# Kernel optimization log

Hardware: AMD Instinct MI355X
Metric: run time of the kernel (lower is better)

The kernel has to match this reference:

```python
import jax, jax.numpy as jnp
import numpy as np

N_VOCAB = 50000
V_SUPPORT = 20000
D = 300
H = 512
B = 8192


def setup_inputs() -> dict:
    key = jax.random.key(0)
    ks = jax.random.split(key, 8)
    ws = jax.random.randint(ks[0], (B,), 0, N_VOCAB, dtype=jnp.int64 if jax.config.jax_enable_x64 else jnp.int32)
    cs = jax.random.randint(ks[1], (B,), 0, N_VOCAB, dtype=ws.dtype)
    vectors = jax.random.normal(ks[2], (N_VOCAB, D), dtype=jnp.float32)
    W1 = jax.random.normal(ks[3], (D, H), dtype=jnp.float32) * (1.0 / np.sqrt(D))
    b1 = jnp.zeros((H,), dtype=jnp.float32)
    W2 = jax.random.normal(ks[4], (H, V_SUPPORT), dtype=jnp.float32) * (1.0 / np.sqrt(H))
    b2 = jnp.zeros((V_SUPPORT,), dtype=jnp.float32)
    vector_to_support = jax.random.randint(ks[5], (N_VOCAB,), 0, V_SUPPORT, dtype=ws.dtype)
    return {"ws": ws, "cs": cs, "vectors": vectors, "W1": W1, "b1": b1,
            "W2": W2, "b2": b2, "vector_to_support": vector_to_support}


def reference(ws, cs, vectors, W1, b1, W2, b2, vector_to_support):
    # embedding lookup of context vectors: [B, D]
    v_c = vectors[cs]
    # FeedForward: Linear -> ReLU -> Linear, then LogSoftmax over support
    h = jax.nn.relu(v_c @ W1 + b1)            # [B, H]
    logits = h @ W2 + b2                       # [B, V]
    logp = jax.nn.log_softmax(logits, axis=-1) # [B, V]
    # map target word (vocab index) -> support index, gather per-row logprob.
    # Original does outputs.T[idx].diag() (O(B^2)); the fused equivalent is a
    # per-row gather: logp[arange(B), idx].
    w_sup = vector_to_support[ws]              # [B]
    logprobs = jnp.take_along_axis(logp, w_sup[:, None], axis=-1)[:, 0]
    return -logprobs                            # [B] NLL per example
```

## Files before the change

kernel.cpp:

```cpp
#include <hip/hip_runtime.h>
#include <hip/hip_bf16.h>
#include <hip/hip_fp8.h>
#include <math.h>


typedef __bf16 bf16x8 __attribute__((ext_vector_type(8)));
typedef float f32x4 __attribute__((ext_vector_type(4)));
typedef int i32x4 __attribute__((ext_vector_type(4)));
typedef int i32x8 __attribute__((ext_vector_type(8)));

#define B_N 8192
#define D_N 300
#define K1K 320
#define H_N 512
#define V_N 20000
#define V_PAD 20480
#define NSPLIT 16
#define SPLIT_V 1280
#define NCH 40
#define ROWS_BLK 128
#define CHUNK_BYTES 16384

#define OFF_PART (8388608u)
#define OFF_W1T  (OFF_PART + 16u*8192u*8u)
#define OFF_B2L  (OFF_W1T + 512u*320u*2u)
#define OFF_H8   (OFF_B2L + 20480u*4u)
#define OFF_W2T8 (OFF_H8 + 8192u*512u)

#define SCALE1 0x7F7F7F7F
#define LOG2E  1.4426950408889634f

__device__ inline unsigned short f2bf(float f) {
  __hip_bfloat16 h = __float2bfloat16(f);
  return *reinterpret_cast<unsigned short*>(&h);
}

__device__ inline unsigned char f2fp8(float f) {
  __hip_fp8_e4m3 q(f);
  return (unsigned char)q.__x;
}

__device__ inline float fp82f(unsigned char b) {
  __hip_fp8_e4m3 q; q.__x = b;
  return (float)q;
}

__device__ __forceinline__ void gl16(const void* g, void* l) {
  __builtin_amdgcn_global_load_lds(
      (const __attribute__((address_space(1))) void*)g,
      (__attribute__((address_space(3))) void*)l, 16, 0, 0);
}

__global__ __launch_bounds__(256) void kprep(
    const float* __restrict__ W2, unsigned long long* __restrict__ W2T8u,
    const float* __restrict__ W1, unsigned int* __restrict__ W1Tu,
    const float* __restrict__ b2, float* __restrict__ b2l)
{
  __shared__ float tile[64][65];
  const int bid = blockIdx.x;
  const int tid = threadIdx.x;

  if (bid < 2560) {
    const int n0 = (bid >> 3) * 64;
    const int k0 = (bid & 7) * 64;
    #pragma unroll
    for (int it = 0; it < 16; ++it) {
      int idx = it * 256 + tid;
      int i = idx >> 6;
      int j = idx & 63;
      float v = 0.f;
      if (n0 + j < V_N) v = W2[(size_t)(k0 + i) * V_N + n0 + j];
      tile[i][j] = v;
    }
    __syncthreads();
    #pragma unroll
    for (int it = 0; it < 2; ++it) {
      int idx = it * 256 + tid;
      int nl = idx >> 3;
      int g8 = (idx & 7) * 8;
      int n = n0 + nl;
      unsigned long long pack = 0;
      #pragma unroll
      for (int j = 0; j < 8; ++j)
        pack |= (unsigned long long)f2fp8(tile[g8 + j][nl]) << (8 * j);
      unsigned kk = (unsigned)(k0 + g8);
      unsigned off = ((unsigned)n * 512u + (kk ^ (((unsigned)n & 15u) << 4)));
      W2T8u[off >> 3] = pack;
    }
  } else if (bid < 2600) {
    const int idx0 = bid - 2560;
    const int n0 = (idx0 & 7) * 64;
    const int k0 = (idx0 >> 3) * 64;
    #pragma unroll
    for (int it = 0; it < 16; ++it) {
      int idx = it * 256 + tid;
      int i = idx >> 6;
      int j = idx & 63;
      float v = 0.f;
      if (k0 + i < D_N) v = W1[(size_t)(k0 + i) * H_N + n0 + j];
      tile[i][j] = v;
    }
    __syncthreads();
    #pragma unroll
    for (int it = 0; it < 8; ++it) {
      int idx = it * 256 + tid;
      int nl = idx >> 5;
      int k = (idx & 31) * 2;
      unsigned int lo = f2bf(tile[k][nl]);
      unsigned int hi = f2bf(tile[k + 1][nl]);
      W1Tu[((size_t)(n0 + nl) * K1K + k0 + k) >> 1] = (hi << 16) | lo;
    }
  } else {
    int i = (bid - 2600) * 256 + tid;
    if (i < V_PAD) b2l[i] = (i < V_N) ? b2[i] * LOG2E : -3.0e37f;
  }
}

__global__ __launch_bounds__(256) void k1_hidden(
    const int* __restrict__ cs, const float* __restrict__ vectors,
    const unsigned short* __restrict__ W1T,
    const float* __restrict__ b1, unsigned char* __restrict__ h8Out)
{
  __shared__ __align__(16) unsigned short vca[16][328];
  __shared__ int rowIdx[16];
  const int tid = threadIdx.x;
  const int lane = tid & 63;
  const int w = tid >> 6;
  const int l15 = lane & 15;
  const int l4 = lane >> 4;
  const int r0 = blockIdx.x * 16;
  if (tid < 16) rowIdx[tid] = cs[r0 + tid];
  __syncthreads();
  for (int idx = tid; idx < 16 * 328; idx += 256) {
    int r = idx / 328;
    int k = idx - r * 328;
    float v = (k < D_N) ? vectors[(size_t)rowIdx[r] * D_N + k] : 0.f;
    vca[r][k] = f2bf(v);
  }
  __syncthreads();

  bf16x8 afr[10];
  #pragma unroll
  for (int t = 0; t < 10; ++t)
    afr[t] = *(const bf16x8*)&vca[l15][t * 32 + l4 * 8];

  f32x4 acc[8];
  #pragma unroll
  for (int ct = 0; ct < 8; ++ct) acc[ct] = (f32x4){0.f, 0.f, 0.f, 0.f};

  #pragma unroll
  for (int t = 0; t < 10; ++t) {
    #pragma unroll
    for (int ct = 0; ct < 8; ++ct) {
      const int n = w * 128 + ct * 16 + l15;
      bf16x8 bfr = *(const bf16x8*)(W1T + (size_t)n * K1K + t * 32 + l4 * 8);
      acc[ct] = __builtin_amdgcn_mfma_f32_16x16x32_bf16(afr[t], bfr, acc[ct], 0, 0, 0);
    }
  }

  #pragma unroll
  for (int ct = 0; ct < 8; ++ct) {
    const int n = w * 128 + ct * 16 + l15;
    const float bb = b1[n];
    #pragma unroll
    for (int r = 0; r < 4; ++r) {
      const int row = r0 + l4 * 4 + r;
      h8Out[(size_t)row * H_N + n] = f2fp8(fmaxf(acc[ct][r] + bb, 0.f));
    }
  }
}

__device__ __forceinline__ void stage_chunk(const char* g, char* l, int tid) {
  #pragma unroll
  for (int it = 0; it < 4; ++it) {
    const unsigned o = (unsigned)tid * 16 + it * 4096;
    gl16(g + o, l + o);
  }
}

__global__ __launch_bounds__(256, 4) void k3_fused(
    const unsigned char* __restrict__ h8,
    const char* __restrict__ W2T8,
    const float* __restrict__ b2l,
    float2* __restrict__ partOut)
{
  __shared__ __align__(16) char smB[2 * CHUNK_BYTES];
  __shared__ float b2s[SPLIT_V];
  const int tid = threadIdx.x;
  const int lane = tid & 63;
  const int w = tid >> 6;
  const int l15 = lane & 15;
  const int l4 = lane >> 4;
  const int s = blockIdx.x & 15;
  const int rb = blockIdx.x >> 4;
  const int r0 = rb * ROWS_BLK + w * 32;
  const char* gsplit = W2T8 + (size_t)s * SPLIT_V * 512;
  const int sCol = s * SPLIT_V;

  i32x8 afr[2][4];
  #pragma unroll
  for (int m = 0; m < 2; ++m) {
    const unsigned char* ap = h8 + (size_t)(r0 + m * 16 + l15) * H_N + l4 * 32;
    #pragma unroll
    for (int t = 0; t < 4; ++t) {
      i32x4 lo = *(const i32x4*)(ap + t * 128);
      i32x4 hi = *(const i32x4*)(ap + t * 128 + 16);
      afr[m][t] = __builtin_shufflevector(lo, hi, 0, 1, 2, 3, 4, 5, 6, 7);
    }
  }

  float s_run[8];
  #pragma unroll
  for (int ri = 0; ri < 8; ++ri) s_run[ri] = 0.f;

  for (int i = tid; i < SPLIT_V; i += 256) b2s[i] = b2l[sCol + i];

  stage_chunk(gsplit, smB, tid);

  const unsigned swz = (unsigned)l15 << 4;

  #pragma unroll 1
  for (int c = 0; c < NCH; ++c) {
    asm volatile("s_waitcnt vmcnt(0) lgkmcnt(0)" ::: "memory");
    __builtin_amdgcn_s_barrier();

    char* cur = smB + (c & 1) * CHUNK_BYTES;
    if (c + 1 < NCH)
      stage_chunk(gsplit + (size_t)(c + 1) * CHUNK_BYTES,
                  smB + ((c & 1) ^ 1) * CHUNK_BYTES, tid);

    const float b2c0 = b2s[c * 32 + l15];
    const float b2c1 = b2s[c * 32 + 16 + l15];

    f32x4 acc[2][2];
    #pragma unroll
    for (int m = 0; m < 2; ++m)
      #pragma unroll
      for (int ct = 0; ct < 2; ++ct) acc[m][ct] = (f32x4){0.f, 0.f, 0.f, 0.f};

    #pragma unroll
    for (int t = 0; t < 4; ++t) {
      const char* bp = cur + l15 * 512;
      i32x4 lo = *(const i32x4*)(bp + (((unsigned)(t * 128 + l4 * 32)) ^ swz));
      i32x4 hi = *(const i32x4*)(bp + (((unsigned)(t * 128 + l4 * 32 + 16)) ^ swz));
      i32x8 bfr = __builtin_shufflevector(lo, hi, 0, 1, 2, 3, 4, 5, 6, 7);
      __builtin_amdgcn_s_setprio(1);
      acc[0][0] = __builtin_amdgcn_mfma_scale_f32_16x16x128_f8f6f4(
          afr[0][t], bfr, acc[0][0], 0, 0, 0, SCALE1, 0, SCALE1);
      acc[1][0] = __builtin_amdgcn_mfma_scale_f32_16x16x128_f8f6f4(
          afr[1][t], bfr, acc[1][0], 0, 0, 0, SCALE1, 0, SCALE1);
      __builtin_amdgcn_s_setprio(0);
    }

    #pragma unroll
    for (int t = 0; t < 4; ++t) {
      const char* bp = cur + (16 + l15) * 512;
      i32x4 lo = *(const i32x4*)(bp + (((unsigned)(t * 128 + l4 * 32)) ^ swz));
      i32x4 hi = *(const i32x4*)(bp + (((unsigned)(t * 128 + l4 * 32 + 16)) ^ swz));
      i32x8 bfr = __builtin_shufflevector(lo, hi, 0, 1, 2, 3, 4, 5, 6, 7);
      __builtin_amdgcn_s_setprio(1);
      acc[0][1] = __builtin_amdgcn_mfma_scale_f32_16x16x128_f8f6f4(
          afr[0][t], bfr, acc[0][1], 0, 0, 0, SCALE1, 0, SCALE1);
      acc[1][1] = __builtin_amdgcn_mfma_scale_f32_16x16x128_f8f6f4(
          afr[1][t], bfr, acc[1][1], 0, 0, 0, SCALE1, 0, SCALE1);
      __builtin_amdgcn_s_setprio(0);
      #pragma unroll
      for (int r2 = 0; r2 < 2; ++r2) {
        const int ri = t * 2 + r2;
        const int m_ = ri >> 2, r_ = ri & 3;
        s_run[ri] += __builtin_amdgcn_exp2f(fmaf(acc[m_][0][r_], LOG2E, b2c0));
      }
    }

    #pragma unroll
    for (int m = 0; m < 2; ++m)
      #pragma unroll
      for (int r = 0; r < 4; ++r)
        s_run[m * 4 + r] += __builtin_amdgcn_exp2f(fmaf(acc[m][1][r], LOG2E, b2c1));
  }

  #pragma unroll
  for (int m = 0; m < 2; ++m)
    #pragma unroll
    for (int r = 0; r < 4; ++r) {
      int ri = m * 4 + r;
      float sc = s_run[ri];
      #pragma unroll
      for (int k = 1; k < 16; k <<= 1) sc += __shfl_xor(sc, k);
      if (l15 == 0) {
        int grow = r0 + m * 16 + l4 * 4 + r;
        partOut[(size_t)s * B_N + grow] = make_float2(0.f, sc);
      }
    }
}

__global__ __launch_bounds__(256) void k45_final(
    const unsigned char* __restrict__ h8, const char* __restrict__ W2T8,
    const float* __restrict__ b2, const int* __restrict__ wsIdx,
    const int* __restrict__ v2s, const float2* __restrict__ part,
    float* __restrict__ out)
{
  const int row = blockIdx.x * 4 + (threadIdx.x >> 6);
  const int lane = threadIdx.x & 63;
  const int tc = v2s[wsIdx[row]];
  unsigned long long hv = *(const unsigned long long*)(h8 + (size_t)row * H_N + lane * 8);
  const unsigned off = ((unsigned)(lane * 8)) ^ (((unsigned)tc & 15u) << 4);
  unsigned long long wv = *(const unsigned long long*)(W2T8 + (size_t)tc * 512 + off);
  float sdot = 0.f;
  #pragma unroll
  for (int j = 0; j < 8; ++j)
    sdot += fp82f((unsigned char)(hv >> (8 * j))) * fp82f((unsigned char)(wv >> (8 * j)));
  #pragma unroll
  for (int k = 32; k >= 1; k >>= 1) sdot += __shfl_xor(sdot, k);
  if (lane == 0) {
    const float tgt = sdot + b2[tc];
    float S = 0.f;
    #pragma unroll
    for (int s = 0; s < NSPLIT; ++s) S += part[(size_t)s * B_N + row].y;
    out[row] = logf(S) - tgt;
  }
}

extern "C" void kernel_launch(void* const* d_in, const int* in_sizes, int n_in,
                              void* d_out, int out_size, void* d_ws, size_t ws_size,
                              hipStream_t stream) {
  const int*   wsIdx   = (const int*)d_in[0];
  const int*   cs      = (const int*)d_in[1];
  const float* vectors = (const float*)d_in[2];
  const float* W1      = (const float*)d_in[3];
  const float* b1      = (const float*)d_in[4];
  const float* W2      = (const float*)d_in[5];
  const float* b2      = (const float*)d_in[6];
  const int*   v2s     = (const int*)d_in[7];

  char* wsb = (char*)d_ws;
  float2* part = (float2*)(wsb + OFF_PART);
  unsigned short* W1T = (unsigned short*)(wsb + OFF_W1T);
  float*  b2l  = (float*)(wsb + OFF_B2L);
  unsigned char* h8   = (unsigned char*)(wsb + OFF_H8);
  char*   W2T8 = wsb + OFF_W2T8;
  float*  out  = (float*)d_out;

  hipLaunchKernelGGL(kprep, dim3(2680), dim3(256), 0, stream,
                     W2, (unsigned long long*)W2T8, W1, (unsigned int*)W1T, b2, b2l);
  hipLaunchKernelGGL(k1_hidden, dim3(B_N / 16), dim3(256), 0, stream, cs, vectors, W1T, b1, h8);
  hipLaunchKernelGGL(k3_fused, dim3((B_N / ROWS_BLK) * NSPLIT), dim3(256), 0, stream,
                     h8, W2T8, b2l, part);
  hipLaunchKernelGGL(k45_final, dim3(B_N / 4), dim3(256), 0, stream,
                     h8, W2T8, b2, wsIdx, v2s, part, out);
}
```

Measured before the change: 123.9 us.

## Read W2 fp8 fragments directly from global memory instead of LDS staging

```diff
diff --git a/kernel.cpp b/kernel.cpp
--- a/kernel.cpp
+++ b/kernel.cpp
@@ -19,7 +19,6 @@
 #define SPLIT_V 1280
 #define NCH 40
 #define ROWS_BLK 128
-#define CHUNK_BYTES 16384
 
 #define OFF_PART (8388608u)
 #define OFF_W1T  (OFF_PART + 16u*8192u*8u)
@@ -43,12 +42,6 @@
 __device__ inline float fp82f(unsigned char b) {
   __hip_fp8_e4m3 q; q.__x = b;
   return (float)q;
-}
-
-__device__ __forceinline__ void gl16(const void* g, void* l) {
-  __builtin_amdgcn_global_load_lds(
-      (const __attribute__((address_space(1))) void*)g,
-      (__attribute__((address_space(3))) void*)l, 16, 0, 0);
 }
 
 __global__ __launch_bounds__(256) void kprep(
@@ -83,8 +76,7 @@
       #pragma unroll
       for (int j = 0; j < 8; ++j)
         pack |= (unsigned long long)f2fp8(tile[g8 + j][nl]) << (8 * j);
-      unsigned kk = (unsigned)(k0 + g8);
-      unsigned off = ((unsigned)n * 512u + (kk ^ (((unsigned)n & 15u) << 4)));
+      unsigned off = ((unsigned)n * 512u + (unsigned)(k0 + g8));
       W2T8u[off >> 3] = pack;
     }
   } else if (bid < 2600) {
@@ -170,22 +162,12 @@
   }
 }
 
-__device__ __forceinline__ void stage_chunk(const char* g, char* l, int tid) {
-  #pragma unroll
-  for (int it = 0; it < 4; ++it) {
-    const unsigned o = (unsigned)tid * 16 + it * 4096;
-    gl16(g + o, l + o);
-  }
-}
-
 __global__ __launch_bounds__(256, 4) void k3_fused(
     const unsigned char* __restrict__ h8,
     const char* __restrict__ W2T8,
     const float* __restrict__ b2l,
     float2* __restrict__ partOut)
 {
-  __shared__ __align__(16) char smB[2 * CHUNK_BYTES];
-  __shared__ float b2s[SPLIT_V];
   const int tid = threadIdx.x;
   const int lane = tid & 63;
   const int w = tid >> 6;
@@ -194,7 +176,6 @@
   const int s = blockIdx.x & 15;
   const int rb = blockIdx.x >> 4;
   const int r0 = rb * ROWS_BLK + w * 32;
-  const char* gsplit = W2T8 + (size_t)s * SPLIT_V * 512;
   const int sCol = s * SPLIT_V;
 
   i32x8 afr[2][4];
@@ -213,24 +194,15 @@
   #pragma unroll
   for (int ri = 0; ri < 8; ++ri) s_run[ri] = 0.f;
 
-  for (int i = tid; i < SPLIT_V; i += 256) b2s[i] = b2l[sCol + i];
-
-  stage_chunk(gsplit, smB, tid);
-
-  const unsigned swz = (unsigned)l15 << 4;
+  const char* bbase = W2T8 + (size_t)(sCol + l15) * 512 + l4 * 32;
 
   #pragma unroll 1
   for (int c = 0; c < NCH; ++c) {
-    asm volatile("s_waitcnt vmcnt(0) lgkmcnt(0)" ::: "memory");
-    __builtin_amdgcn_s_barrier();
-
-    char* cur = smB + (c & 1) * CHUNK_BYTES;
-    if (c + 1 < NCH)
-      stage_chunk(gsplit + (size_t)(c + 1) * CHUNK_BYTES,
-                  smB + ((c & 1) ^ 1) * CHUNK_BYTES, tid);
-
-    const float b2c0 = b2s[c * 32 + l15];
-    const float b2c1 = b2s[c * 32 + 16 + l15];
+    const float b2c0 = b2l[sCol + c * 32 + l15];
+    const float b2c1 = b2l[sCol + c * 32 + 16 + l15];
+
+    const char* bp0 = bbase + (size_t)(c * 32) * 512;
+    const char* bp1 = bp0 + 16 * 512;
 
     f32x4 acc[2][2];
     #pragma unroll
@@ -240,9 +212,8 @@
 
     #pragma unroll
     for (int t = 0; t < 4; ++t) {
-      const char* bp = cur + l15 * 512;
-      i32x4 lo = *(const i32x4*)(bp + (((unsigned)(t * 128 + l4 * 32)) ^ swz));
-      i32x4 hi = *(const i32x4*)(bp + (((unsigned)(t * 128 + l4 * 32 + 16)) ^ swz));
+      i32x4 lo = *(const i32x4*)(bp0 + t * 128);
+      i32x4 hi = *(const i32x4*)(bp0 + t * 128 + 16);
       i32x8 bfr = __builtin_shufflevector(lo, hi, 0, 1, 2, 3, 4, 5, 6, 7);
       __builtin_amdgcn_s_setprio(1);
       acc[0][0] = __builtin_amdgcn_mfma_scale_f32_16x16x128_f8f6f4(
@@ -254,9 +225,8 @@
 
     #pragma unroll
     for (int t = 0; t < 4; ++t) {
-      const char* bp = cur + (16 + l15) * 512;
-      i32x4 lo = *(const i32x4*)(bp + (((unsigned)(t * 128 + l4 * 32)) ^ swz));
-      i32x4 hi = *(const i32x4*)(bp + (((unsigned)(t * 128 + l4 * 32 + 16)) ^ swz));
+      i32x4 lo = *(const i32x4*)(bp1 + t * 128);
+      i32x4 hi = *(const i32x4*)(bp1 + t * 128 + 16);
       i32x8 bfr = __builtin_shufflevector(lo, hi, 0, 1, 2, 3, 4, 5, 6, 7);
       __builtin_amdgcn_s_setprio(1);
       acc[0][1] = __builtin_amdgcn_mfma_scale_f32_16x16x128_f8f6f4(
@@ -304,8 +274,7 @@
   const int lane = threadIdx.x & 63;
   const int tc = v2s[wsIdx[row]];
   unsigned long long hv = *(const unsigned long long*)(h8 + (size_t)row * H_N + lane * 8);
-  const unsigned off = ((unsigned)(lane * 8)) ^ (((unsigned)tc & 15u) << 4);
-  unsigned long long wv = *(const unsigned long long*)(W2T8 + (size_t)tc * 512 + off);
+  unsigned long long wv = *(const unsigned long long*)(W2T8 + (size_t)tc * 512 + lane * 8);
   float sdot = 0.f;
   #pragma unroll
   for (int j = 0; j < 8; ++j)
```

Result: slower. 340.3 us (+174.6%).

## Load second half of W2 chunk directly into registers from fragment-ordered copy

Applied to the files above, without the earlier changes.

```diff
diff --git a/kernel.cpp b/kernel.cpp
--- a/kernel.cpp
+++ b/kernel.cpp
@@ -20,7 +20,9 @@
 #define NCH 40
 #define ROWS_BLK 128
 #define CHUNK_BYTES 16384
-
+#define STG_BYTES 8192
+
+#define OFF_W2F  0u
 #define OFF_PART (8388608u)
 #define OFF_W1T  (OFF_PART + 16u*8192u*8u)
 #define OFF_B2L  (OFF_W1T + 512u*320u*2u)
@@ -53,6 +55,7 @@
 
 __global__ __launch_bounds__(256) void kprep(
     const float* __restrict__ W2, unsigned long long* __restrict__ W2T8u,
+    unsigned long long* __restrict__ W2Fu,
     const float* __restrict__ W1, unsigned int* __restrict__ W1Tu,
     const float* __restrict__ b2, float* __restrict__ b2l)
 {
@@ -86,6 +89,14 @@
       unsigned kk = (unsigned)(k0 + g8);
       unsigned off = ((unsigned)n * 512u + (kk ^ (((unsigned)n & 15u) << 4)));
       W2T8u[off >> 3] = pack;
+      if (n & 16) {
+        unsigned sc = (unsigned)n >> 5;
+        unsigned t  = kk >> 7;
+        unsigned l4 = (kk >> 5) & 3;
+        unsigned lanei = l4 * 16 + ((unsigned)n & 15);
+        unsigned foff = (((sc * 4 + t) * 64) + lanei) * 32 + (kk & 31);
+        W2Fu[foff >> 3] = pack;
+      }
     }
   } else if (bid < 2600) {
     const int idx0 = bid - 2560;
@@ -170,9 +181,9 @@
   }
 }
 
-__device__ __forceinline__ void stage_chunk(const char* g, char* l, int tid) {
-  #pragma unroll
-  for (int it = 0; it < 4; ++it) {
+__device__ __forceinline__ void stage_half(const char* g, char* l, int tid) {
+  #pragma unroll
+  for (int it = 0; it < 2; ++it) {
     const unsigned o = (unsigned)tid * 16 + it * 4096;
     gl16(g + o, l + o);
   }
@@ -181,10 +192,11 @@
 __global__ __launch_bounds__(256, 4) void k3_fused(
     const unsigned char* __restrict__ h8,
     const char* __restrict__ W2T8,
+    const char* __restrict__ W2F,
     const float* __restrict__ b2l,
     float2* __restrict__ partOut)
 {
-  __shared__ __align__(16) char smB[2 * CHUNK_BYTES];
+  __shared__ __align__(16) char smB[2 * STG_BYTES];
   __shared__ float b2s[SPLIT_V];
   const int tid = threadIdx.x;
   const int lane = tid & 63;
@@ -195,6 +207,7 @@
   const int rb = blockIdx.x >> 4;
   const int r0 = rb * ROWS_BLK + w * 32;
   const char* gsplit = W2T8 + (size_t)s * SPLIT_V * 512;
+  const char* fsplit = W2F + ((size_t)s * NCH * 4 * 64) * 32 + (size_t)lane * 32;
   const int sCol = s * SPLIT_V;
 
   i32x8 afr[2][4];
@@ -215,7 +228,7 @@
 
   for (int i = tid; i < SPLIT_V; i += 256) b2s[i] = b2l[sCol + i];
 
-  stage_chunk(gsplit, smB, tid);
+  stage_half(gsplit, smB, tid);
 
   const unsigned swz = (unsigned)l15 << 4;
 
@@ -224,10 +237,20 @@
     asm volatile("s_waitcnt vmcnt(0) lgkmcnt(0)" ::: "memory");
     __builtin_amdgcn_s_barrier();
 
-    char* cur = smB + (c & 1) * CHUNK_BYTES;
+    const char* fb = fsplit + (size_t)(c * 4) * 2048;
+    i32x4 dlo0 = *(const i32x4*)(fb);
+    i32x4 dhi0 = *(const i32x4*)(fb + 16);
+    i32x4 dlo1 = *(const i32x4*)(fb + 2048);
+    i32x4 dhi1 = *(const i32x4*)(fb + 2048 + 16);
+    i32x4 dlo2 = *(const i32x4*)(fb + 2 * 2048);
+    i32x4 dhi2 = *(const i32x4*)(fb + 2 * 2048 + 16);
+    i32x4 dlo3 = *(const i32x4*)(fb + 3 * 2048);
+    i32x4 dhi3 = *(const i32x4*)(fb + 3 * 2048 + 16);
+
+    char* cur = smB + (c & 1) * STG_BYTES;
     if (c + 1 < NCH)
-      stage_chunk(gsplit + (size_t)(c + 1) * CHUNK_BYTES,
-                  smB + ((c & 1) ^ 1) * CHUNK_BYTES, tid);
+      stage_half(gsplit + (size_t)(c + 1) * CHUNK_BYTES,
+                 smB + ((c & 1) ^ 1) * STG_BYTES, tid);
 
     const float b2c0 = b2s[c * 32 + l15];
     const float b2c1 = b2s[c * 32 + 16 + l15];
@@ -254,9 +277,8 @@
 
     #pragma unroll
     for (int t = 0; t < 4; ++t) {
-      const char* bp = cur + (16 + l15) * 512;
-      i32x4 lo = *(const i32x4*)(bp + (((unsigned)(t * 128 + l4 * 32)) ^ swz));
-      i32x4 hi = *(const i32x4*)(bp + (((unsigned)(t * 128 + l4 * 32 + 16)) ^ swz));
+      i32x4 lo = (t == 0) ? dlo0 : (t == 1) ? dlo1 : (t == 2) ? dlo2 : dlo3;
+      i32x4 hi = (t == 0) ? dhi0 : (t == 1) ? dhi1 : (t == 2) ? dhi2 : dhi3;
       i32x8 bfr = __builtin_shufflevector(lo, hi, 0, 1, 2, 3, 4, 5, 6, 7);
       __builtin_amdgcn_s_setprio(1);
       acc[0][1] = __builtin_amdgcn_mfma_scale_f32_16x16x128_f8f6f4(
@@ -334,6 +356,7 @@
   const int*   v2s     = (const int*)d_in[7];
 
   char* wsb = (char*)d_ws;
+  char*   W2F  = wsb + OFF_W2F;
   float2* part = (float2*)(wsb + OFF_PART);
   unsigned short* W1T = (unsigned short*)(wsb + OFF_W1T);
   float*  b2l  = (float*)(wsb + OFF_B2L);
@@ -342,10 +365,11 @@
   float*  out  = (float*)d_out;
 
   hipLaunchKernelGGL(kprep, dim3(2680), dim3(256), 0, stream,
-                     W2, (unsigned long long*)W2T8, W1, (unsigned int*)W1T, b2, b2l);
+                     W2, (unsigned long long*)W2T8, (unsigned long long*)W2F,
+                     W1, (unsigned int*)W1T, b2, b2l);
   hipLaunchKernelGGL(k1_hidden, dim3(B_N / 16), dim3(256), 0, stream, cs, vectors, W1T, b1, h8);
   hipLaunchKernelGGL(k3_fused, dim3((B_N / ROWS_BLK) * NSPLIT), dim3(256), 0, stream,
-                     h8, W2T8, b2l, part);
+                     h8, W2T8, W2F, b2l, part);
   hipLaunchKernelGGL(k45_final, dim3(B_N / 4), dim3(256), 0, stream,
                      h8, W2T8, b2, wsIdx, v2s, part, out);
 }
```

New measurement: 306.2 us. +147.2%, slower.
